# Kernel tuning notes

Hardware: AMD Instinct MI355X
Metric: run time of the kernel (lower is better)

Reference implementation:

```python
import jax, jax.numpy as jnp
import numpy as np

H, C = 4, 64            # heads, hidden_channels (per-head dim, concat=False)
N_SRC = N_TGT = 50000
E = 400000
E_LBL = 200000
NEG_SLOPE = 0.2
LN_EPS = 1e-5


def _gatv2(x_src, x_dst, ei, Wl, bl, Wr, br, att, bias, n_dst):
    # PyG GATv2Conv, bipartite, add_self_loops=False, concat=False (mean over heads)
    xl = (x_src @ Wl.T + bl).reshape(x_src.shape[0], H, C)   # lin_l(x_src)
    xr = (x_dst @ Wr.T + br).reshape(x_dst.shape[0], H, C)   # lin_r(x_dst)
    s, d = ei[0], ei[1]
    e = jax.nn.leaky_relu(xl[s] + xr[d], NEG_SLOPE)          # [E,H,C]
    logits = jnp.einsum('ehc,hc->eh', e, att)                # [E,H]
    m = jax.ops.segment_max(logits, d, num_segments=n_dst)
    m = jnp.where(jnp.isfinite(m), m, 0.0)                   # empty segments -> 0
    ex = jnp.exp(logits - m[d])
    den = jax.ops.segment_sum(ex, d, num_segments=n_dst)
    alpha = ex / (den[d] + 1e-16)                            # segment softmax over dst
    out = jax.ops.segment_sum(xl[s] * alpha[:, :, None], d, num_segments=n_dst)
    return out.mean(axis=1) + bias                           # [n_dst, C]


def _layer_norm(x, w, b):
    mu = x.mean(-1, keepdims=True)
    v = ((x - mu) ** 2).mean(-1, keepdims=True)
    return (x - mu) / jnp.sqrt(v + LN_EPS) * w + b


def setup_inputs() -> dict:
    key = jax.random.key(0)
    ks = iter(jax.random.split(key, 64))
    def p(shape, scale=0.1):
        return jax.random.normal(next(ks), shape, jnp.float32) * scale
    inp = {}
    inp['src_emb'] = p((N_SRC, C))
    inp['tgt_emb'] = p((N_TGT, C))
    for name in ['c1st', 'c1ts', 'c2st', 'c2ts']:
        inp[name + '_Wl'] = p((H * C, C))
        inp[name + '_bl'] = jnp.zeros((H * C,), jnp.float32)
        inp[name + '_Wr'] = p((H * C, C))
        inp[name + '_br'] = jnp.zeros((H * C,), jnp.float32)
        inp[name + '_att'] = p((H, C))
        inp[name + '_bias'] = jnp.zeros((C,), jnp.float32)
    inp['ln_s_w'] = jnp.ones((C,), jnp.float32)
    inp['ln_s_b'] = jnp.zeros((C,), jnp.float32)
    inp['ln_t_w'] = jnp.ones((C,), jnp.float32)
    inp['ln_t_b'] = jnp.zeros((C,), jnp.float32)
    inp['node_id_source'] = jnp.arange(N_SRC)
    inp['node_id_target'] = jnp.arange(N_TGT)
    inp['edge_index_st'] = jax.random.randint(next(ks), (2, E), 0, N_SRC)
    inp['edge_index_ts'] = jax.random.randint(next(ks), (2, E), 0, N_TGT)
    inp['edge_label_index'] = jax.random.randint(next(ks), (2, E_LBL), 0, N_SRC)
    return inp


def reference(src_emb, tgt_emb,
              c1st_Wl, c1st_bl, c1st_Wr, c1st_br, c1st_att, c1st_bias,
              c1ts_Wl, c1ts_bl, c1ts_Wr, c1ts_br, c1ts_att, c1ts_bias,
              c2st_Wl, c2st_bl, c2st_Wr, c2st_br, c2st_att, c2st_bias,
              c2ts_Wl, c2ts_bl, c2ts_Wr, c2ts_br, c2ts_att, c2ts_bias,
              ln_s_w, ln_s_b, ln_t_w, ln_t_b,
              node_id_source, node_id_target,
              edge_index_st, edge_index_ts, edge_label_index):
    x_s = src_emb[node_id_source]
    x_t = tgt_emb[node_id_target]
    # layer 1 (to_hetero: one conv per edge type, sum-aggregate per node type)
    h_t = _gatv2(x_s, x_t, edge_index_st, c1st_Wl, c1st_bl, c1st_Wr, c1st_br, c1st_att, c1st_bias, N_TGT)
    h_s = _gatv2(x_t, x_s, edge_index_ts, c1ts_Wl, c1ts_bl, c1ts_Wr, c1ts_br, c1ts_att, c1ts_bias, N_SRC)
    h_s = _layer_norm(jax.nn.relu(h_s), ln_s_w, ln_s_b)
    h_t = _layer_norm(jax.nn.relu(h_t), ln_t_w, ln_t_b)
    # layer 2
    o_t = _gatv2(h_s, h_t, edge_index_st, c2st_Wl, c2st_bl, c2st_Wr, c2st_br, c2st_att, c2st_bias, N_TGT)
    o_s = _gatv2(h_t, h_s, edge_index_ts, c2ts_Wl, c2ts_bl, c2ts_Wr, c2ts_br, c2ts_att, c2ts_bias, N_SRC)
    # classifier: edge-wise dot product
    pred = (o_s[edge_label_index[0]] * o_t[edge_label_index[1]]).sum(axis=-1)
    return pred
```

## Files before the change

kernel.cpp:

```cpp
#include <hip/hip_runtime.h>

#define NEG_SLOPE 0.2f
#define LN_EPS 1e-5f
#define LOG2E 1.44269504088896f

typedef __attribute__((ext_vector_type(8))) short bf16x8;
typedef __attribute__((ext_vector_type(4))) float f32x4;
typedef __attribute__((ext_vector_type(2))) float f32x2;

__device__ __forceinline__ short f2bf(float f) {
    unsigned u = __float_as_uint(f);
    return (short)((u + 0x7FFFu + ((u >> 16) & 1u)) >> 16);
}

#define DPP_ADD(v, ctrl) \
    v += __int_as_float(__builtin_amdgcn_update_dpp(0, __float_as_int(v), ctrl, 0xF, 0xF, true))
__device__ __forceinline__ float dpp_sum16(float v) {
    DPP_ADD(v, 0xB1);
    DPP_ADD(v, 0x4E);
    DPP_ADD(v, 0x141);
    DPP_ADD(v, 0x140);
    return v;
}

__device__ __forceinline__ void unpack4(uint2 w, f32x2& lo, f32x2& hi) {
    lo.x = __uint_as_float(w.x << 16);
    lo.y = __uint_as_float(w.x & 0xFFFF0000u);
    hi.x = __uint_as_float(w.y << 16);
    hi.y = __uint_as_float(w.y & 0xFFFF0000u);
}

struct WSrc8 { const float* s[8]; };
__global__ __launch_bounds__(256) void wprep_kernel(WSrc8 W, unsigned short* dst)
{
    int gidx = blockIdx.x * 256 + threadIdx.x;
    int mid = gidx >> 12;
    int within = (gidx & 4095) * 4;
    float4 v = *(const float4*)(W.s[mid] + within);
    ushort4 o;
    o.x = (unsigned short)f2bf(v.x);
    o.y = (unsigned short)f2bf(v.y);
    o.z = (unsigned short)f2bf(v.z);
    o.w = (unsigned short)f2bf(v.w);
    *(ushort4*)(dst + mid * 16384 + within) = o;
}

struct LinJob {
    const void* x; const int* ids; const unsigned short* Wb; const float* bias;
    unsigned short* out; int n; int xbf16;
};
struct LinJob4 { LinJob j[4]; };

__global__ __launch_bounds__(256) void lin4_kernel(LinJob4 P, int bpj)
{
    int jid = blockIdx.x / bpj;
    LinJob job = P.j[jid];
    int blk = blockIdx.x - jid * bpj;
    const int* __restrict__ ids = job.ids;
    int n = job.n;

    int wv = threadIdx.x >> 6;
    int lane = threadIdx.x & 63;
    int m = lane & 15, q = lane >> 4;
    bf16x8 wfrag[4][2];
#pragma unroll
    for (int t = 0; t < 4; ++t) {
        int ncol = wv * 64 + t * 16 + m;
        const unsigned short* wr = job.Wb + ncol * 64 + q * 8;
#pragma unroll
        for (int h = 0; h < 2; ++h)
            wfrag[t][h] = *(const bf16x8*)(wr + h * 32);
    }
    float4 biasv[4];
#pragma unroll
    for (int t = 0; t < 4; ++t)
        biasv[t] = *(const float4*)(job.bias + wv * 64 + t * 16 + q * 4);

    int ntiles = (n + 15) >> 4;
    for (int tile = blk; tile < ntiles; tile += bpj) {
        int row = tile * 16 + m;
        int rc = row < n ? row : n - 1;
        int src = ids ? ids[rc] : rc;
        bf16x8 xfrag[2];
        if (job.xbf16) {
            const unsigned short* xr = (const unsigned short*)job.x + (size_t)src * 64 + q * 8;
#pragma unroll
            for (int h = 0; h < 2; ++h)
                xfrag[h] = *(const bf16x8*)(xr + h * 32);
        } else {
            const float* xr = (const float*)job.x + (size_t)src * 64 + q * 8;
#pragma unroll
            for (int h = 0; h < 2; ++h) {
                const float4* p = (const float4*)(xr + h * 32);
                float4 u = p[0], v = p[1];
                bf16x8 f;
                f[0]=f2bf(u.x); f[1]=f2bf(u.y); f[2]=f2bf(u.z); f[3]=f2bf(u.w);
                f[4]=f2bf(v.x); f[5]=f2bf(v.y); f[6]=f2bf(v.z); f[7]=f2bf(v.w);
                xfrag[h] = f;
            }
        }
        bool valid = row < n;
        unsigned short* orow = job.out + (size_t)row * 256 + wv * 64 + q * 4;
#pragma unroll
        for (int t = 0; t < 4; ++t) {
            f32x4 acc = {0.f, 0.f, 0.f, 0.f};
            acc = __builtin_amdgcn_mfma_f32_16x16x32_bf16(wfrag[t][0], xfrag[0], acc, 0, 0, 0);
            acc = __builtin_amdgcn_mfma_f32_16x16x32_bf16(wfrag[t][1], xfrag[1], acc, 0, 0, 0);
            if (valid) {
                ushort4 o;
                o.x = (unsigned short)f2bf(acc[0] + biasv[t].x);
                o.y = (unsigned short)f2bf(acc[1] + biasv[t].y);
                o.z = (unsigned short)f2bf(acc[2] + biasv[t].z);
                o.w = (unsigned short)f2bf(acc[3] + biasv[t].w);
                *(ushort4*)(orow + t * 16) = o;
            }
        }
    }
}

__global__ __launch_bounds__(256) void hist2_kernel(
    const int* __restrict__ ed0, int E0, int* __restrict__ cnt0,
    const int* __restrict__ ed1, int E1, int* __restrict__ cnt1)
{
    int i = blockIdx.x * 256 + threadIdx.x;
    if (i < E0) atomicAdd(&cnt0[ed0[i]], 1);
    else { int k = i - E0; if (k < E1) atomicAdd(&cnt1[ed1[k]], 1); }
}

__global__ __launch_bounds__(256) void chunk_sum2_kernel(
    const int* __restrict__ cnt0, int* __restrict__ csum0, int n0, int nc0,
    const int* __restrict__ cnt1, int* __restrict__ csum1, int n1)
{
    const int* cnt; int* csum; int n; int blk;
    if (blockIdx.x < (unsigned)nc0) { cnt = cnt0; csum = csum0; n = n0; blk = blockIdx.x; }
    else { cnt = cnt1; csum = csum1; n = n1; blk = blockIdx.x - nc0; }
    __shared__ int wsm[4];
    int tid = threadIdx.x;
    int base = blk * 1024 + tid * 4;
    int s = 0;
#pragma unroll
    for (int k = 0; k < 4; ++k) { int i = base + k; if (i < n) s += cnt[i]; }
#pragma unroll
    for (int ofs = 32; ofs > 0; ofs >>= 1) s += __shfl_xor(s, ofs, 64);
    if ((tid & 63) == 0) wsm[tid >> 6] = s;
    __syncthreads();
    if (tid == 0) csum[blk] = wsm[0] + wsm[1] + wsm[2] + wsm[3];
}

__global__ __launch_bounds__(128) void chunk_scan2_kernel(
    int* __restrict__ c0, int n0, int* __restrict__ c1, int n1)
{
    int w = threadIdx.x >> 6, lane = threadIdx.x & 63;
    int* c = w ? c1 : c0;
    int n = w ? n1 : n0;
    int v = (lane < n) ? c[lane] : 0;
    int incl = v;
#pragma unroll
    for (int ofs = 1; ofs < 64; ofs <<= 1) {
        int t = __shfl_up(incl, ofs, 64);
        if (lane >= ofs) incl += t;
    }
    if (lane < n) c[lane] = incl - v;
}

__global__ __launch_bounds__(1024) void scan_apply2_kernel(
    const int* __restrict__ cnt0, const int* __restrict__ co0, int* __restrict__ offs0, int n0, int nc0,
    const int* __restrict__ cnt1, const int* __restrict__ co1, int* __restrict__ offs1, int n1)
{
    const int* cnt; const int* co; int* offs; int n; int blk;
    if (blockIdx.x < (unsigned)nc0) { cnt = cnt0; co = co0; offs = offs0; n = n0; blk = blockIdx.x; }
    else { cnt = cnt1; co = co1; offs = offs1; n = n1; blk = blockIdx.x - nc0; }
    __shared__ int wsum[16];
    int tid = threadIdx.x, lane = tid & 63, w = tid >> 6;
    int i = blk * 1024 + tid;
    int v = (i < n) ? cnt[i] : 0;
    int incl = v;
#pragma unroll
    for (int ofs = 1; ofs < 64; ofs <<= 1) {
        int t = __shfl_up(incl, ofs, 64);
        if (lane >= ofs) incl += t;
    }
    if (lane == 63) wsum[w] = incl;
    __syncthreads();
    if (w == 0) {
        int x = (lane < 16) ? wsum[lane] : 0;
#pragma unroll
        for (int ofs = 1; ofs < 16; ofs <<= 1) {
            int t = __shfl_up(x, ofs, 64);
            if (lane >= ofs) x += t;
        }
        if (lane < 16) wsum[lane] = x;
    }
    __syncthreads();
    int woff = (w == 0) ? 0 : wsum[w - 1];
    if (i < n) offs[i + 1] = co[blk] + woff + incl;
    if (i == 0) offs[0] = 0;
}

__global__ __launch_bounds__(256) void fill2_kernel(
    const int* __restrict__ es0, const int* __restrict__ ed0,
    const int* __restrict__ offs0, int* __restrict__ cur0, int* __restrict__ srt0, int E0,
    const int* __restrict__ es1, const int* __restrict__ ed1,
    const int* __restrict__ offs1, int* __restrict__ cur1, int* __restrict__ srt1, int E1)
{
    int i = blockIdx.x * 256 + threadIdx.x;
    if (i < E0) {
        int d = ed0[i];
        int pos = offs0[d] + atomicAdd(&cur0[d], 1);
        srt0[pos] = es0[i];
    } else {
        int k = i - E0;
        if (k < E1) {
            int d = ed1[k];
            int pos = offs1[d] + atomicAdd(&cur1[d], 1);
            srt1[pos] = es1[k];
        }
    }
}

struct GatJob {
    const unsigned short* A; const unsigned short* B;
    const int* offs; const int* srt;
    const float* att; const float* bias;
    const float* lnw; const float* lnb;
    unsigned short* out; int n_dst;
};

__global__ __launch_bounds__(256) void gat2_kernel(GatJob j0, GatJob j1, int blocks0)
{
    GatJob job = (blockIdx.x < (unsigned)blocks0) ? j0 : j1;
    int blk = (blockIdx.x < (unsigned)blocks0) ? blockIdx.x : blockIdx.x - blocks0;
    int d = blk * 4 + (threadIdx.x >> 6);
    int lane = threadIdx.x & 63;
    if (d >= job.n_dst) return;
    int g = lane & 15;
    const uint2* __restrict__ A2 = (const uint2*)job.A;
    float4 att4 = ((const float4*)job.att)[lane];
    f32x2 att01 = {att4.x * LOG2E, att4.y * LOG2E};
    f32x2 att23 = {att4.z * LOG2E, att4.w * LOG2E};
    uint2 bw = ((const uint2*)(job.B + (size_t)d * 256))[lane];
    f32x2 b01, b23; unpack4(bw, b01, b23);
    const f32x2 z2 = {0.f, 0.f};

    float den1 = 0.f, den2 = 0.f;
    f32x2 p01 = z2, p23 = z2, q01 = z2, q23 = z2;
    const int* __restrict__ srt = job.srt;
    int j0i = __builtin_amdgcn_readfirstlane(job.offs[d]);
    int j1i = __builtin_amdgcn_readfirstlane(job.offs[d + 1]);
    int j = j0i;

#define EDGE(S, DEN, A01, A23) { \
        const uint2* rowp = A2 + (size_t)(S) * 64;    \
        uint2 wbits = rowp[lane];                     \
        f32x2 a01, a23; unpack4(wbits, a01, a23); \
        f32x2 t01 = a01 + b01, t23 = a23 + b23; \
        f32x2 l01 = __builtin_elementwise_max(t01 * NEG_SLOPE, t01); \
        f32x2 l23 = __builtin_elementwise_max(t23 * NEG_SLOPE, t23); \
        f32x2 dp = l01 * att01 + l23 * att23; \
        float p = dpp_sum16(dp.x + dp.y); \
        float pe = __builtin_amdgcn_exp2f(p); \
        DEN += pe; \
        A01 = a01 * pe + A01; \
        A23 = a23 * pe + A23; }

    for (; j + 1 < j1i; j += 2) {
        int s0 = __builtin_amdgcn_readfirstlane(srt[j]);
        int s1 = __builtin_amdgcn_readfirstlane(srt[j + 1]);
        EDGE(s0, den1, p01, p23)
        EDGE(s1, den2, q01, q23)
    }
    if (j < j1i) {
        int s0 = __builtin_amdgcn_readfirstlane(srt[j]);
        EDGE(s0, den1, p01, p23)
    }
#undef EDGE

    float den = den1 + den2;
    f32x2 A01 = p01 + q01, A23 = p23 + q23;
    float inv = 1.f / (den + 1e-16f);
    A01 *= inv; A23 *= inv;
    float4 acc = {A01.x, A01.y, A23.x, A23.y};
    acc.x += __shfl_xor(acc.x, 16, 64);
    acc.y += __shfl_xor(acc.y, 16, 64);
    acc.z += __shfl_xor(acc.z, 16, 64);
    acc.w += __shfl_xor(acc.w, 16, 64);
    acc.x += __shfl_xor(acc.x, 32, 64);
    acc.y += __shfl_xor(acc.y, 32, 64);
    acc.z += __shfl_xor(acc.z, 32, 64);
    acc.w += __shfl_xor(acc.w, 32, 64);
    float4 b4 = ((const float4*)job.bias)[g];
    float4 v;
    v.x = acc.x * 0.25f + b4.x;
    v.y = acc.y * 0.25f + b4.y;
    v.z = acc.z * 0.25f + b4.z;
    v.w = acc.w * 0.25f + b4.w;
    if (job.lnw) {
        v.x = v.x > 0.f ? v.x : 0.f;
        v.y = v.y > 0.f ? v.y : 0.f;
        v.z = v.z > 0.f ? v.z : 0.f;
        v.w = v.w > 0.f ? v.w : 0.f;
        float s  = dpp_sum16(v.x + v.y + v.z + v.w);
        float ss = dpp_sum16(v.x*v.x + v.y*v.y + v.z*v.z + v.w*v.w);
        float mu = s * (1.f / 64.f);
        float var = ss * (1.f / 64.f) - mu * mu;
        float rs = rsqrtf(var + LN_EPS);
        float4 w4 = ((const float4*)job.lnw)[g];
        float4 l4 = ((const float4*)job.lnb)[g];
        v.x = (v.x - mu) * rs * w4.x + l4.x;
        v.y = (v.y - mu) * rs * w4.y + l4.y;
        v.z = (v.z - mu) * rs * w4.z + l4.z;
        v.w = (v.w - mu) * rs * w4.w + l4.w;
    }
    if (lane < 16) {
        ushort4 o;
        o.x = (unsigned short)f2bf(v.x);
        o.y = (unsigned short)f2bf(v.y);
        o.z = (unsigned short)f2bf(v.z);
        o.w = (unsigned short)f2bf(v.w);
        *(ushort4*)(job.out + (size_t)d * 64 + g * 4) = o;
    }
}

__global__ __launch_bounds__(256) void dot_kernel(
    const unsigned short* __restrict__ os, const unsigned short* __restrict__ ot,
    const int* __restrict__ ea, const int* __restrict__ eb,
    float* __restrict__ out, int n)
{
    int e = (int)((blockIdx.x * 256u + threadIdx.x) >> 4);
    int l = threadIdx.x & 15;
    if (e >= n) return;
    uint2 aw = ((const uint2*)(os + (size_t)ea[e] * 64))[l];
    uint2 bw = ((const uint2*)(ot + (size_t)eb[e] * 64))[l];
    f32x2 a01, a23, b01, b23;
    unpack4(aw, a01, a23);
    unpack4(bw, b01, b23);
    f32x2 dp = a01 * b01 + a23 * b23;
    float v = dpp_sum16(dp.x + dp.y);
    if (l == 0) out[e] = v;
}

extern "C" void kernel_launch(void* const* d_in, const int* in_sizes, int n_in,
                              void* d_out, int out_size, void* d_ws, size_t ws_size,
                              hipStream_t stream)
{
    const float* src_emb = (const float*)d_in[0];
    const float* tgt_emb = (const float*)d_in[1];
    const float* P[4][6];
    for (int ci = 0; ci < 4; ++ci)
        for (int k = 0; k < 6; ++k)
            P[ci][k] = (const float*)d_in[2 + ci * 6 + k];
    const float* ln_s_w = (const float*)d_in[26];
    const float* ln_s_b = (const float*)d_in[27];
    const float* ln_t_w = (const float*)d_in[28];
    const float* ln_t_b = (const float*)d_in[29];
    const int* nid_s = (const int*)d_in[30];
    const int* nid_t = (const int*)d_in[31];
    const int* ei_st = (const int*)d_in[32];
    const int* ei_ts = (const int*)d_in[33];
    const int* eli   = (const int*)d_in[34];

    int n_src = in_sizes[30];
    int n_tgt = in_sizes[31];
    int E_st = in_sizes[32] / 2;
    int E_ts = in_sizes[33] / 2;
    int EL   = in_sizes[34] / 2;
    int nmax = n_src > n_tgt ? n_src : n_tgt;

    float* ws = (float*)d_ws;
    size_t off = 0;
    auto alloc = [&](size_t count) {
        float* p = ws + off;
        off += (count + 63) & ~(size_t)63;
        return p;
    };
    unsigned short* A_st = (unsigned short*)alloc((size_t)nmax * 128);
    unsigned short* B_st = (unsigned short*)alloc((size_t)nmax * 128);
    unsigned short* A_ts = (unsigned short*)alloc((size_t)nmax * 128);
    unsigned short* B_ts = (unsigned short*)alloc((size_t)nmax * 128);
    unsigned short* Wbf  = (unsigned short*)alloc(65536);
    int*   offs_st = (int*)alloc((size_t)n_tgt + 1);
    int*   srt_st  = (int*)alloc((size_t)E_st);
    int*   offs_ts = (int*)alloc((size_t)n_src + 1);
    int*   srt_ts  = (int*)alloc((size_t)E_ts);
    int*   zeros   = (int*)alloc((size_t)4 * nmax);
    int*   csum0   = (int*)alloc(64);
    int*   csum1   = (int*)alloc(64);
    unsigned short* h_s = (unsigned short*)alloc((size_t)n_src * 32);
    unsigned short* h_t = (unsigned short*)alloc((size_t)n_tgt * 32);
    unsigned short* o_s = (unsigned short*)alloc((size_t)n_src * 32);
    unsigned short* o_t = (unsigned short*)alloc((size_t)n_tgt * 32);
    if (off * sizeof(float) > ws_size) return;

    int* cnt0 = zeros;
    int* cnt1 = zeros + nmax;
    int* cur0 = zeros + 2 * (size_t)nmax;
    int* cur1 = zeros + 3 * (size_t)nmax;

    WSrc8 WS;
    for (int ci = 0; ci < 4; ++ci) { WS.s[ci*2] = P[ci][0]; WS.s[ci*2+1] = P[ci][2]; }
    wprep_kernel<<<128, 256, 0, stream>>>(WS, Wbf);

    int nc0 = (n_tgt + 1023) / 1024, nc1 = (n_src + 1023) / 1024;
    hipMemsetAsync(zeros, 0, (size_t)4 * nmax * sizeof(int), stream);
    hist2_kernel<<<(E_st + E_ts + 255) / 256, 256, 0, stream>>>(
        ei_st + E_st, E_st, cnt0, ei_ts + E_ts, E_ts, cnt1);
    chunk_sum2_kernel<<<nc0 + nc1, 256, 0, stream>>>(cnt0, csum0, n_tgt, nc0, cnt1, csum1, n_src);
    chunk_scan2_kernel<<<1, 128, 0, stream>>>(csum0, nc0, csum1, nc1);
    scan_apply2_kernel<<<nc0 + nc1, 1024, 0, stream>>>(
        cnt0, csum0, offs_st, n_tgt, nc0, cnt1, csum1, offs_ts, n_src);
    fill2_kernel<<<(E_st + E_ts + 255) / 256, 256, 0, stream>>>(
        ei_st, ei_st + E_st, offs_st, cur0, srt_st, E_st,
        ei_ts, ei_ts + E_ts, offs_ts, cur1, srt_ts, E_ts);

    int bpj = 256;

    auto lin_layer = [&](const void* xs, const int* ids_s, int ns,
                         const void* xt, const int* ids_t, int nt, int xbf,
                         int slot_base,
                         const float* const* pst, const float* const* pts) {
        LinJob4 LJ;
        LJ.j[0] = { xs, ids_s, Wbf + (slot_base+0)*16384, pst[1], A_st, ns, xbf };
        LJ.j[1] = { xt, ids_t, Wbf + (slot_base+1)*16384, pst[3], B_st, nt, xbf };
        LJ.j[2] = { xt, ids_t, Wbf + (slot_base+2)*16384, pts[1], A_ts, nt, xbf };
        LJ.j[3] = { xs, ids_s, Wbf + (slot_base+3)*16384, pts[3], B_ts, ns, xbf };
        lin4_kernel<<<4 * bpj, 256, 0, stream>>>(LJ, bpj);
    };
    auto gat_layer = [&](const float* const* pst, const float* const* pts,
                         const float* lnw_t, const float* lnb_t,
                         const float* lnw_s, const float* lnb_s,
                         unsigned short* out_t, unsigned short* out_s) {
        GatJob g0 = { A_st, B_st, offs_st, srt_st, pst[4], pst[5], lnw_t, lnb_t, out_t, n_tgt };
        GatJob g1 = { A_ts, B_ts, offs_ts, srt_ts, pts[4], pts[5], lnw_s, lnb_s, out_s, n_src };
        int b0 = (n_tgt + 3) / 4, b1 = (n_src + 3) / 4;
        gat2_kernel<<<b0 + b1, 256, 0, stream>>>(g0, g1, b0);
    };

    lin_layer(src_emb, nid_s, n_src, tgt_emb, nid_t, n_tgt, 0, 0, P[0], P[1]);
    gat_layer(P[0], P[1], ln_t_w, ln_t_b, ln_s_w, ln_s_b, h_t, h_s);

    lin_layer(h_s, nullptr, n_src, h_t, nullptr, n_tgt, 1, 4, P[2], P[3]);
    gat_layer(P[2], P[3], nullptr, nullptr, nullptr, nullptr, o_t, o_s);

    dot_kernel<<<((size_t)EL * 16 + 255) / 256, 256, 0, stream>>>(
        o_s, o_t, eli, eli + EL, (float*)d_out, EL);
}
```

Measured before the change: 439.7 us.

## Pre-convert embeddings to bf16 in prep kernel and process two row tiles per iteration

The weight-prep kernel now also converts the src and tgt fp32 embedding tables to bf16 once, so the first-layer linear kernel reads bf16 like the second layer, and the runtime dtype branch is removed. The lin4 kernel now processes two 16-row tiles per loop iteration to get more independent loads and MFMAs in flight. The embedding pre-pass costs an extra full read and write of both tables, while the lin kernels read half as many bytes per row and have one code path.

```diff
diff --git a/kernel.cpp b/kernel.cpp
--- a/kernel.cpp
+++ b/kernel.cpp
@@ -31,23 +31,34 @@
 }
 
 struct WSrc8 { const float* s[8]; };
-__global__ __launch_bounds__(256) void wprep_kernel(WSrc8 W, unsigned short* dst)
-{
-    int gidx = blockIdx.x * 256 + threadIdx.x;
-    int mid = gidx >> 12;
-    int within = (gidx & 4095) * 4;
-    float4 v = *(const float4*)(W.s[mid] + within);
+__global__ __launch_bounds__(256) void prep_kernel(
+    WSrc8 W, unsigned short* wdst,
+    const float* e0, unsigned short* d0, int nb0,
+    const float* e1, unsigned short* d1, int nb1)
+{
+    const float* src; unsigned short* dst; int idx;
+    if (blockIdx.x < 128) {
+        int gidx = blockIdx.x * 256 + threadIdx.x;
+        int mid = gidx >> 12;
+        src = W.s[mid]; dst = wdst + mid * 16384;
+        idx = (gidx & 4095);
+    } else if (blockIdx.x < (unsigned)(128 + nb0)) {
+        src = e0; dst = d0; idx = (blockIdx.x - 128) * 256 + threadIdx.x;
+    } else {
+        src = e1; dst = d1; idx = (blockIdx.x - 128 - nb0) * 256 + threadIdx.x;
+    }
+    float4 v = *(const float4*)(src + idx * 4);
     ushort4 o;
     o.x = (unsigned short)f2bf(v.x);
     o.y = (unsigned short)f2bf(v.y);
     o.z = (unsigned short)f2bf(v.z);
     o.w = (unsigned short)f2bf(v.w);
-    *(ushort4*)(dst + mid * 16384 + within) = o;
+    *(ushort4*)(dst + idx * 4) = o;
 }
 
 struct LinJob {
-    const void* x; const int* ids; const unsigned short* Wb; const float* bias;
-    unsigned short* out; int n; int xbf16;
+    const unsigned short* x; const int* ids; const unsigned short* Wb;
+    const float* bias; unsigned short* out; int n;
 };
 struct LinJob4 { LinJob j[4]; };
 
@@ -57,6 +68,7 @@
     LinJob job = P.j[jid];
     int blk = blockIdx.x - jid * bpj;
     const int* __restrict__ ids = job.ids;
+    const unsigned short* __restrict__ x = job.x;
     int n = job.n;
 
     int wv = threadIdx.x >> 6;
@@ -65,8 +77,7 @@
     bf16x8 wfrag[4][2];
 #pragma unroll
     for (int t = 0; t < 4; ++t) {
-        int ncol = wv * 64 + t * 16 + m;
-        const unsigned short* wr = job.Wb + ncol * 64 + q * 8;
+        const unsigned short* wr = job.Wb + (wv * 64 + t * 16 + m) * 64 + q * 8;
 #pragma unroll
         for (int h = 0; h < 2; ++h)
             wfrag[t][h] = *(const bf16x8*)(wr + h * 32);
@@ -77,42 +88,46 @@
         biasv[t] = *(const float4*)(job.bias + wv * 64 + t * 16 + q * 4);
 
     int ntiles = (n + 15) >> 4;
-    for (int tile = blk; tile < ntiles; tile += bpj) {
-        int row = tile * 16 + m;
-        int rc = row < n ? row : n - 1;
-        int src = ids ? ids[rc] : rc;
-        bf16x8 xfrag[2];
-        if (job.xbf16) {
-            const unsigned short* xr = (const unsigned short*)job.x + (size_t)src * 64 + q * 8;
-#pragma unroll
-            for (int h = 0; h < 2; ++h)
-                xfrag[h] = *(const bf16x8*)(xr + h * 32);
-        } else {
-            const float* xr = (const float*)job.x + (size_t)src * 64 + q * 8;
-#pragma unroll
-            for (int h = 0; h < 2; ++h) {
-                const float4* p = (const float4*)(xr + h * 32);
-                float4 u = p[0], v = p[1];
-                bf16x8 f;
-                f[0]=f2bf(u.x); f[1]=f2bf(u.y); f[2]=f2bf(u.z); f[3]=f2bf(u.w);
-                f[4]=f2bf(v.x); f[5]=f2bf(v.y); f[6]=f2bf(v.z); f[7]=f2bf(v.w);
-                xfrag[h] = f;
+    for (int t0 = blk * 2; t0 < ntiles; t0 += bpj * 2) {
+        int t1 = (t0 + 1 < ntiles) ? t0 + 1 : t0;
+        int rowA = t0 * 16 + m, rowB = t1 * 16 + m;
+        int rA = rowA < n ? rowA : n - 1;
+        int rB = rowB < n ? rowB : n - 1;
+        int sA = ids ? ids[rA] : rA;
+        int sB = ids ? ids[rB] : rB;
+        const unsigned short* xrA = x + (size_t)sA * 64 + q * 8;
+        const unsigned short* xrB = x + (size_t)sB * 64 + q * 8;
+        bf16x8 xfA[2], xfB[2];
+        xfA[0] = *(const bf16x8*)(xrA);
+        xfA[1] = *(const bf16x8*)(xrA + 32);
+        xfB[0] = *(const bf16x8*)(xrB);
+        xfB[1] = *(const bf16x8*)(xrB + 32);
+        bool vA = rowA < n, vB = (rowB < n) && (t1 != t0);
+        unsigned short* oA = job.out + (size_t)rowA * 256 + wv * 64 + q * 4;
+        unsigned short* oB = job.out + (size_t)rowB * 256 + wv * 64 + q * 4;
+#pragma unroll
+        for (int t = 0; t < 4; ++t) {
+            f32x4 accA = {0.f, 0.f, 0.f, 0.f};
+            accA = __builtin_amdgcn_mfma_f32_16x16x32_bf16(wfrag[t][0], xfA[0], accA, 0, 0, 0);
+            accA = __builtin_amdgcn_mfma_f32_16x16x32_bf16(wfrag[t][1], xfA[1], accA, 0, 0, 0);
+            f32x4 accB = {0.f, 0.f, 0.f, 0.f};
+            accB = __builtin_amdgcn_mfma_f32_16x16x32_bf16(wfrag[t][0], xfB[0], accB, 0, 0, 0);
+            accB = __builtin_amdgcn_mfma_f32_16x16x32_bf16(wfrag[t][1], xfB[1], accB, 0, 0, 0);
+            if (vA) {
+                ushort4 o;
+                o.x = (unsigned short)f2bf(accA[0] + biasv[t].x);
+                o.y = (unsigned short)f2bf(accA[1] + biasv[t].y);
+                o.z = (unsigned short)f2bf(accA[2] + biasv[t].z);
+                o.w = (unsigned short)f2bf(accA[3] + biasv[t].w);
+                *(ushort4*)(oA + t * 16) = o;
             }
-        }
-        bool valid = row < n;
-        unsigned short* orow = job.out + (size_t)row * 256 + wv * 64 + q * 4;
-#pragma unroll
-        for (int t = 0; t < 4; ++t) {
-            f32x4 acc = {0.f, 0.f, 0.f, 0.f};
-            acc = __builtin_amdgcn_mfma_f32_16x16x32_bf16(wfrag[t][0], xfrag[0], acc, 0, 0, 0);
-            acc = __builtin_amdgcn_mfma_f32_16x16x32_bf16(wfrag[t][1], xfrag[1], acc, 0, 0, 0);
-            if (valid) {
+            if (vB) {
                 ushort4 o;
-                o.x = (unsigned short)f2bf(acc[0] + biasv[t].x);
-                o.y = (unsigned short)f2bf(acc[1] + biasv[t].y);
-                o.z = (unsigned short)f2bf(acc[2] + biasv[t].z);
-                o.w = (unsigned short)f2bf(acc[3] + biasv[t].w);
-                *(ushort4*)(orow + t * 16) = o;
+                o.x = (unsigned short)f2bf(accB[0] + biasv[t].x);
+                o.y = (unsigned short)f2bf(accB[1] + biasv[t].y);
+                o.z = (unsigned short)f2bf(accB[2] + biasv[t].z);
+                o.w = (unsigned short)f2bf(accB[3] + biasv[t].w);
+                *(ushort4*)(oB + t * 16) = o;
             }
         }
     }
@@ -378,6 +393,8 @@
     unsigned short* A_ts = (unsigned short*)alloc((size_t)nmax * 128);
     unsigned short* B_ts = (unsigned short*)alloc((size_t)nmax * 128);
     unsigned short* Wbf  = (unsigned short*)alloc(65536);
+    unsigned short* e_s = (unsigned short*)alloc((size_t)n_src * 32);
+    unsigned short* e_t = (unsigned short*)alloc((size_t)n_tgt * 32);
     int*   offs_st = (int*)alloc((size_t)n_tgt + 1);
     int*   srt_st  = (int*)alloc((size_t)E_st);
     int*   offs_ts = (int*)alloc((size_t)n_src + 1);
@@ -398,7 +415,10 @@
 
     WSrc8 WS;
     for (int ci = 0; ci < 4; ++ci) { WS.s[ci*2] = P[ci][0]; WS.s[ci*2+1] = P[ci][2]; }
-    wprep_kernel<<<128, 256, 0, stream>>>(WS, Wbf);
+    int nb0 = (n_src * 64 / 4 + 255) / 256;
+    int nb1 = (n_tgt * 64 / 4 + 255) / 256;
+    prep_kernel<<<128 + nb0 + nb1, 256, 0, stream>>>(
+        WS, Wbf, src_emb, e_s, nb0, tgt_emb, e_t, nb1);
 
     int nc0 = (n_tgt + 1023) / 1024, nc1 = (n_src + 1023) / 1024;
     hipMemsetAsync(zeros, 0, (size_t)4 * nmax * sizeof(int), stream);
@@ -414,15 +434,15 @@
 
     int bpj = 256;
 
-    auto lin_layer = [&](const void* xs, const int* ids_s, int ns,
-                         const void* xt, const int* ids_t, int nt, int xbf,
+    auto lin_layer = [&](const unsigned short* xs, const int* ids_s, int ns,
+                         const unsigned short* xt, const int* ids_t, int nt,
                          int slot_base,
                          const float* const* pst, const float* const* pts) {
         LinJob4 LJ;
-        LJ.j[0] = { xs, ids_s, Wbf + (slot_base+0)*16384, pst[1], A_st, ns, xbf };
-        LJ.j[1] = { xt, ids_t, Wbf + (slot_base+1)*16384, pst[3], B_st, nt, xbf };
-        LJ.j[2] = { xt, ids_t, Wbf + (slot_base+2)*16384, pts[1], A_ts, nt, xbf };
-        LJ.j[3] = { xs, ids_s, Wbf + (slot_base+3)*16384, pts[3], B_ts, ns, xbf };
+        LJ.j[0] = { xs, ids_s, Wbf + (slot_base+0)*16384, pst[1], A_st, ns };
+        LJ.j[1] = { xt, ids_t, Wbf + (slot_base+1)*16384, pst[3], B_st, nt };
+        LJ.j[2] = { xt, ids_t, Wbf + (slot_base+2)*16384, pts[1], A_ts, nt };
+        LJ.j[3] = { xs, ids_s, Wbf + (slot_base+3)*16384, pts[3], B_ts, ns };
         lin4_kernel<<<4 * bpj, 256, 0, stream>>>(LJ, bpj);
     };
     auto gat_layer = [&](const float* const* pst, const float* const* pts,
@@ -435,10 +455,10 @@
         gat2_kernel<<<b0 + b1, 256, 0, stream>>>(g0, g1, b0);
     };
 
-    lin_layer(src_emb, nid_s, n_src, tgt_emb, nid_t, n_tgt, 0, 0, P[0], P[1]);
+    lin_layer(e_s, nid_s, n_src, e_t, nid_t, n_tgt, 0, P[0], P[1]);
     gat_layer(P[0], P[1], ln_t_w, ln_t_b, ln_s_w, ln_s_b, h_t, h_s);
 
-    lin_layer(h_s, nullptr, n_src, h_t, nullptr, n_tgt, 1, 4, P[2], P[3]);
+    lin_layer(h_s, nullptr, n_src, h_t, nullptr, n_tgt, 4, P[2], P[3]);
     gat_layer(P[2], P[3], nullptr, nullptr, nullptr, nullptr, o_t, o_s);
 
     dot_kernel<<<((size_t)EL * 16 + 255) / 256, 256, 0, stream>>>(
```

After: 450.5 us. 1.02x slower.

## Switch intermediate storage and edge math from bf16/fp32 to packed fp16

Applied to the files above, without the earlier changes.

Replaces bf16 storage with fp16 everywhere: weights and embeddings are converted to fp16 in one prep kernel, the linear layers use fp16 MFMA, and the GAT edge loop runs on packed half2 arithmetic with fdot2 dot products and fp16 accumulators. This cuts the unpack and convert instructions in the edge-bound inner loop and the in-kernel fp32 to bf16 conversion in layer 1. The cost is an extra prep pass over the embeddings and reduced precision and range, since softmax-weighted sums now accumulate in fp16. The fdot2 seed constant -0.375 shifts every logit; the shift cancels in the softmax, but it is an odd addition.

```diff
diff --git a/kernel.cpp b/kernel.cpp
--- a/kernel.cpp
+++ b/kernel.cpp
@@ -4,13 +4,17 @@
 #define LN_EPS 1e-5f
 #define LOG2E 1.44269504088896f
 
-typedef __attribute__((ext_vector_type(8))) short bf16x8;
+typedef __attribute__((ext_vector_type(2))) _Float16 h16x2;
+typedef __attribute__((ext_vector_type(8))) _Float16 h16x8;
 typedef __attribute__((ext_vector_type(4))) float f32x4;
-typedef __attribute__((ext_vector_type(2))) float f32x2;
-
-__device__ __forceinline__ short f2bf(float f) {
-    unsigned u = __float_as_uint(f);
-    return (short)((u + 0x7FFFu + ((u >> 16) & 1u)) >> 16);
+
+__device__ __forceinline__ h16x2 u2h(unsigned u) { return __builtin_bit_cast(h16x2, u); }
+__device__ __forceinline__ unsigned h2u(h16x2 h) { return __builtin_bit_cast(unsigned, h); }
+__device__ __forceinline__ unsigned pk(float a, float b) {
+    return __builtin_bit_cast(unsigned, __builtin_amdgcn_cvt_pkrtz(a, b));
+}
+__device__ __forceinline__ h16x2 pkh(float a, float b) {
+    return __builtin_bit_cast(h16x2, __builtin_amdgcn_cvt_pkrtz(a, b));
 }
 
 #define DPP_ADD(v, ctrl) \
@@ -23,31 +27,34 @@
     return v;
 }
 
-__device__ __forceinline__ void unpack4(uint2 w, f32x2& lo, f32x2& hi) {
-    lo.x = __uint_as_float(w.x << 16);
-    lo.y = __uint_as_float(w.x & 0xFFFF0000u);
-    hi.x = __uint_as_float(w.y << 16);
-    hi.y = __uint_as_float(w.y & 0xFFFF0000u);
-}
-
 struct WSrc8 { const float* s[8]; };
-__global__ __launch_bounds__(256) void wprep_kernel(WSrc8 W, unsigned short* dst)
-{
-    int gidx = blockIdx.x * 256 + threadIdx.x;
-    int mid = gidx >> 12;
-    int within = (gidx & 4095) * 4;
-    float4 v = *(const float4*)(W.s[mid] + within);
-    ushort4 o;
-    o.x = (unsigned short)f2bf(v.x);
-    o.y = (unsigned short)f2bf(v.y);
-    o.z = (unsigned short)f2bf(v.z);
-    o.w = (unsigned short)f2bf(v.w);
-    *(ushort4*)(dst + mid * 16384 + within) = o;
+__global__ __launch_bounds__(256) void prep_kernel(
+    WSrc8 W, unsigned short* wdst,
+    const float* e0, unsigned short* d0, int n0,
+    const float* e1, unsigned short* d1, int nb0)
+{
+    const float* src; unsigned short* dst; int idx; int lim;
+    if (blockIdx.x < 128) {
+        int gidx = blockIdx.x * 256 + threadIdx.x;
+        int mid = gidx >> 12;
+        src = W.s[mid]; dst = wdst + mid * 16384;
+        idx = (gidx & 4095); lim = 4096;
+    } else if (blockIdx.x < (unsigned)(128 + nb0)) {
+        src = e0; dst = d0; idx = (blockIdx.x - 128) * 256 + threadIdx.x; lim = n0 * 16;
+    } else {
+        src = e1; dst = d1; idx = (blockIdx.x - 128 - nb0) * 256 + threadIdx.x; lim = 1 << 30;
+    }
+    if (idx >= lim) return;
+    float4 v = *(const float4*)(src + idx * 4);
+    uint2 o;
+    o.x = pk(v.x, v.y);
+    o.y = pk(v.z, v.w);
+    *(uint2*)(dst + idx * 4) = o;
 }
 
 struct LinJob {
-    const void* x; const int* ids; const unsigned short* Wb; const float* bias;
-    unsigned short* out; int n; int xbf16;
+    const unsigned short* x; const int* ids; const unsigned short* Wh;
+    const float* bias; unsigned short* out; int n;
 };
 struct LinJob4 { LinJob j[4]; };
 
@@ -57,19 +64,19 @@
     LinJob job = P.j[jid];
     int blk = blockIdx.x - jid * bpj;
     const int* __restrict__ ids = job.ids;
+    const unsigned short* __restrict__ x = job.x;
     int n = job.n;
 
     int wv = threadIdx.x >> 6;
     int lane = threadIdx.x & 63;
     int m = lane & 15, q = lane >> 4;
-    bf16x8 wfrag[4][2];
+    h16x8 wfrag[4][2];
 #pragma unroll
     for (int t = 0; t < 4; ++t) {
-        int ncol = wv * 64 + t * 16 + m;
-        const unsigned short* wr = job.Wb + ncol * 64 + q * 8;
+        const unsigned short* wr = job.Wh + (wv * 64 + t * 16 + m) * 64 + q * 8;
 #pragma unroll
         for (int h = 0; h < 2; ++h)
-            wfrag[t][h] = *(const bf16x8*)(wr + h * 32);
+            wfrag[t][h] = *(const h16x8*)(wr + h * 32);
     }
     float4 biasv[4];
 #pragma unroll
@@ -81,38 +88,22 @@
         int row = tile * 16 + m;
         int rc = row < n ? row : n - 1;
         int src = ids ? ids[rc] : rc;
-        bf16x8 xfrag[2];
-        if (job.xbf16) {
-            const unsigned short* xr = (const unsigned short*)job.x + (size_t)src * 64 + q * 8;
-#pragma unroll
-            for (int h = 0; h < 2; ++h)
-                xfrag[h] = *(const bf16x8*)(xr + h * 32);
-        } else {
-            const float* xr = (const float*)job.x + (size_t)src * 64 + q * 8;
-#pragma unroll
-            for (int h = 0; h < 2; ++h) {
-                const float4* p = (const float4*)(xr + h * 32);
-                float4 u = p[0], v = p[1];
-                bf16x8 f;
-                f[0]=f2bf(u.x); f[1]=f2bf(u.y); f[2]=f2bf(u.z); f[3]=f2bf(u.w);
-                f[4]=f2bf(v.x); f[5]=f2bf(v.y); f[6]=f2bf(v.z); f[7]=f2bf(v.w);
-                xfrag[h] = f;
-            }
-        }
+        const unsigned short* xr = x + (size_t)src * 64 + q * 8;
+        h16x8 xfrag[2];
+        xfrag[0] = *(const h16x8*)(xr);
+        xfrag[1] = *(const h16x8*)(xr + 32);
         bool valid = row < n;
         unsigned short* orow = job.out + (size_t)row * 256 + wv * 64 + q * 4;
 #pragma unroll
         for (int t = 0; t < 4; ++t) {
             f32x4 acc = {0.f, 0.f, 0.f, 0.f};
-            acc = __builtin_amdgcn_mfma_f32_16x16x32_bf16(wfrag[t][0], xfrag[0], acc, 0, 0, 0);
-            acc = __builtin_amdgcn_mfma_f32_16x16x32_bf16(wfrag[t][1], xfrag[1], acc, 0, 0, 0);
+            acc = __builtin_amdgcn_mfma_f32_16x16x32_f16(wfrag[t][0], xfrag[0], acc, 0, 0, 0);
+            acc = __builtin_amdgcn_mfma_f32_16x16x32_f16(wfrag[t][1], xfrag[1], acc, 0, 0, 0);
             if (valid) {
-                ushort4 o;
-                o.x = (unsigned short)f2bf(acc[0] + biasv[t].x);
-                o.y = (unsigned short)f2bf(acc[1] + biasv[t].y);
-                o.z = (unsigned short)f2bf(acc[2] + biasv[t].z);
-                o.w = (unsigned short)f2bf(acc[3] + biasv[t].w);
-                *(ushort4*)(orow + t * 16) = o;
+                uint2 o;
+                o.x = pk(acc[0] + biasv[t].x, acc[1] + biasv[t].y);
+                o.y = pk(acc[2] + biasv[t].z, acc[3] + biasv[t].w);
+                *(uint2*)(orow + t * 16) = o;
             }
         }
     }
@@ -236,14 +227,15 @@
     int g = lane & 15;
     const uint2* __restrict__ A2 = (const uint2*)job.A;
     float4 att4 = ((const float4*)job.att)[lane];
-    f32x2 att01 = {att4.x * LOG2E, att4.y * LOG2E};
-    f32x2 att23 = {att4.z * LOG2E, att4.w * LOG2E};
+    h16x2 att01 = pkh(att4.x * LOG2E, att4.y * LOG2E);
+    h16x2 att23 = pkh(att4.z * LOG2E, att4.w * LOG2E);
     uint2 bw = ((const uint2*)(job.B + (size_t)d * 256))[lane];
-    f32x2 b01, b23; unpack4(bw, b01, b23);
-    const f32x2 z2 = {0.f, 0.f};
+    h16x2 b01 = u2h(bw.x), b23 = u2h(bw.y);
+    const h16x2 zh = {(_Float16)0.f, (_Float16)0.f};
+    const h16x2 ns = {(_Float16)NEG_SLOPE, (_Float16)NEG_SLOPE};
 
     float den1 = 0.f, den2 = 0.f;
-    f32x2 p01 = z2, p23 = z2, q01 = z2, q23 = z2;
+    h16x2 p01 = zh, p23 = zh, q01 = zh, q23 = zh;
     const int* __restrict__ srt = job.srt;
     int j0i = __builtin_amdgcn_readfirstlane(job.offs[d]);
     int j1i = __builtin_amdgcn_readfirstlane(job.offs[d + 1]);
@@ -252,16 +244,18 @@
 #define EDGE(S, DEN, A01, A23) { \
         const uint2* rowp = A2 + (size_t)(S) * 64;    \
         uint2 wbits = rowp[lane];                     \
-        f32x2 a01, a23; unpack4(wbits, a01, a23); \
-        f32x2 t01 = a01 + b01, t23 = a23 + b23; \
-        f32x2 l01 = __builtin_elementwise_max(t01 * NEG_SLOPE, t01); \
-        f32x2 l23 = __builtin_elementwise_max(t23 * NEG_SLOPE, t23); \
-        f32x2 dp = l01 * att01 + l23 * att23; \
-        float p = dpp_sum16(dp.x + dp.y); \
+        h16x2 a01 = u2h(wbits.x), a23 = u2h(wbits.y); \
+        h16x2 t01 = a01 + b01, t23 = a23 + b23; \
+        h16x2 l01 = __builtin_elementwise_max(t01 * ns, t01); \
+        h16x2 l23 = __builtin_elementwise_max(t23 * ns, t23); \
+        float p = __builtin_amdgcn_fdot2(l23, att23, \
+                    __builtin_amdgcn_fdot2(l01, att01, -0.375f, false), false); \
+        p = dpp_sum16(p);                             \
         float pe = __builtin_amdgcn_exp2f(p); \
         DEN += pe; \
-        A01 = a01 * pe + A01; \
-        A23 = a23 * pe + A23; }
+        h16x2 peh = pkh(pe, pe); \
+        A01 = a01 * peh + A01; \
+        A23 = a23 * peh + A23; }
 
     for (; j + 1 < j1i; j += 2) {
         int s0 = __builtin_amdgcn_readfirstlane(srt[j]);
@@ -276,10 +270,13 @@
 #undef EDGE
 
     float den = den1 + den2;
-    f32x2 A01 = p01 + q01, A23 = p23 + q23;
+    h16x2 A01 = p01 + q01, A23 = p23 + q23;
     float inv = 1.f / (den + 1e-16f);
-    A01 *= inv; A23 *= inv;
-    float4 acc = {A01.x, A01.y, A23.x, A23.y};
+    float4 acc;
+    acc.x = (float)A01.x * inv;
+    acc.y = (float)A01.y * inv;
+    acc.z = (float)A23.x * inv;
+    acc.w = (float)A23.y * inv;
     acc.x += __shfl_xor(acc.x, 16, 64);
     acc.y += __shfl_xor(acc.y, 16, 64);
     acc.z += __shfl_xor(acc.z, 16, 64);
@@ -312,12 +309,10 @@
         v.w = (v.w - mu) * rs * w4.w + l4.w;
     }
     if (lane < 16) {
-        ushort4 o;
-        o.x = (unsigned short)f2bf(v.x);
-        o.y = (unsigned short)f2bf(v.y);
-        o.z = (unsigned short)f2bf(v.z);
-        o.w = (unsigned short)f2bf(v.w);
-        *(ushort4*)(job.out + (size_t)d * 64 + g * 4) = o;
+        uint2 o;
+        o.x = pk(v.x, v.y);
+        o.y = pk(v.z, v.w);
+        *(uint2*)(job.out + (size_t)d * 64 + g * 4) = o;
     }
 }
 
@@ -331,11 +326,9 @@
     if (e >= n) return;
     uint2 aw = ((const uint2*)(os + (size_t)ea[e] * 64))[l];
     uint2 bw = ((const uint2*)(ot + (size_t)eb[e] * 64))[l];
-    f32x2 a01, a23, b01, b23;
-    unpack4(aw, a01, a23);
-    unpack4(bw, b01, b23);
-    f32x2 dp = a01 * b01 + a23 * b23;
-    float v = dpp_sum16(dp.x + dp.y);
+    float v = __builtin_amdgcn_fdot2(u2h(aw.y), u2h(bw.y),
+                __builtin_amdgcn_fdot2(u2h(aw.x), u2h(bw.x), 0.f, false), false);
+    v = dpp_sum16(v);
     if (l == 0) out[e] = v;
 }
 
@@ -377,7 +370,9 @@
     unsigned short* B_st = (unsigned short*)alloc((size_t)nmax * 128);
     unsigned short* A_ts = (unsigned short*)alloc((size_t)nmax * 128);
     unsigned short* B_ts = (unsigned short*)alloc((size_t)nmax * 128);
-    unsigned short* Wbf  = (unsigned short*)alloc(65536);
+    unsigned short* Whf  = (unsigned short*)alloc(65536);
+    unsigned short* e_s = (unsigned short*)alloc((size_t)n_src * 32);
+    unsigned short* e_t = (unsigned short*)alloc((size_t)n_tgt * 32);
     int*   offs_st = (int*)alloc((size_t)n_tgt + 1);
     int*   srt_st  = (int*)alloc((size_t)E_st);
     int*   offs_ts = (int*)alloc((size_t)n_src + 1);
@@ -398,7 +393,10 @@
 
     WSrc8 WS;
     for (int ci = 0; ci < 4; ++ci) { WS.s[ci*2] = P[ci][0]; WS.s[ci*2+1] = P[ci][2]; }
-    wprep_kernel<<<128, 256, 0, stream>>>(WS, Wbf);
+    int nb0 = (n_src * 16 + 255) / 256;
+    int nb1 = (n_tgt * 16 + 255) / 256;
+    prep_kernel<<<128 + nb0 + nb1, 256, 0, stream>>>(
+        WS, Whf, src_emb, e_s, n_src, tgt_emb, e_t, nb0);
 
     int nc0 = (n_tgt + 1023) / 1024, nc1 = (n_src + 1023) / 1024;
     hipMemsetAsync(zeros, 0, (size_t)4 * nmax * sizeof(int), stream);
@@ -414,15 +412,15 @@
 
     int bpj = 256;
 
-    auto lin_layer = [&](const void* xs, const int* ids_s, int ns,
-                         const void* xt, const int* ids_t, int nt, int xbf,
+    auto lin_layer = [&](const unsigned short* xs, const int* ids_s, int ns,
+                         const unsigned short* xt, const int* ids_t, int nt,
                          int slot_base,
                          const float* const* pst, const float* const* pts) {
         LinJob4 LJ;
-        LJ.j[0] = { xs, ids_s, Wbf + (slot_base+0)*16384, pst[1], A_st, ns, xbf };
-        LJ.j[1] = { xt, ids_t, Wbf + (slot_base+1)*16384, pst[3], B_st, nt, xbf };
-        LJ.j[2] = { xt, ids_t, Wbf + (slot_base+2)*16384, pts[1], A_ts, nt, xbf };
-        LJ.j[3] = { xs, ids_s, Wbf + (slot_base+3)*16384, pts[3], B_ts, ns, xbf };
+        LJ.j[0] = { xs, ids_s, Whf + (slot_base+0)*16384, pst[1], A_st, ns };
+        LJ.j[1] = { xt, ids_t, Whf + (slot_base+1)*16384, pst[3], B_st, nt };
+        LJ.j[2] = { xt, ids_t, Whf + (slot_base+2)*16384, pts[1], A_ts, nt };
+        LJ.j[3] = { xs, ids_s, Whf + (slot_base+3)*16384, pts[3], B_ts, ns };
         lin4_kernel<<<4 * bpj, 256, 0, stream>>>(LJ, bpj);
     };
     auto gat_layer = [&](const float* const* pst, const float* const* pts,
@@ -435,10 +433,10 @@
         gat2_kernel<<<b0 + b1, 256, 0, stream>>>(g0, g1, b0);
     };
 
-    lin_layer(src_emb, nid_s, n_src, tgt_emb, nid_t, n_tgt, 0, 0, P[0], P[1]);
+    lin_layer(e_s, nid_s, n_src, e_t, nid_t, n_tgt, 0, P[0], P[1]);
     gat_layer(P[0], P[1], ln_t_w, ln_t_b, ln_s_w, ln_s_b, h_t, h_s);
 
-    lin_layer(h_s, nullptr, n_src, h_t, nullptr, n_tgt, 1, 4, P[2], P[3]);
+    lin_layer(h_s, nullptr, n_src, h_t, nullptr, n_tgt, 4, P[2], P[3]);
     gat_layer(P[2], P[3], nullptr, nullptr, nullptr, nullptr, o_t, o_s);
 
     dot_kernel<<<((size_t)EL * 16 + 255) / 256, 256, 0, stream>>>(
```

Measured after the change: 439.2 us. Within noise of the previous version (-0.1%).
